# Kernel optimization log

Hardware: AMD Instinct MI355X
Metric: run time of the kernel (lower is better)

## Reference

```python
import jax, jax.numpy as jnp
import numpy as np

P_MIN = 0.8        # minimum cumulative probability mass kept per row
THRESHOLD = 1e-10  # drop matches with probability below this
EPS = 1e-6         # distance clamp (matches dist.clamp(min=1e-6) in backward)

B, N, M, D = 4, 4096, 4096, 3


def setup_inputs() -> dict:
    key = jax.random.key(0)
    kx, ky = jax.random.split(key)
    x = jax.random.normal(kx, (B, N, D), dtype=jnp.float32)
    y = jax.random.normal(ky, (B, M, D), dtype=jnp.float32)
    return {"x": x, "y": y}


def _pairwise_dist(x, y):
    # ||x_i - y_j|| via Gram trick; avoids materializing [B,N,M,D] diff tensor.
    sq = (
        jnp.sum(x * x, axis=-1)[:, :, None]
        + jnp.sum(y * y, axis=-1)[:, None, :]
        - 2.0 * jnp.einsum("bnd,bmd->bnm", x, y)
    )
    return jnp.sqrt(jnp.maximum(sq, EPS * EPS))  # [B, N, M]


def _sparse_match_weights(d):
    # Row-wise soft matching probabilities over targets j.
    p = jax.nn.softmax(-d, axis=-1)  # [B, N, M]
    # Keep the most-probable entries per row until cumulative mass reaches P_MIN
    # (the dense, jit-friendly equivalent of the COO compaction in the kernel).
    order = jnp.argsort(-p, axis=-1)
    p_sorted = jnp.take_along_axis(p, order, axis=-1)
    csum = jnp.cumsum(p_sorted, axis=-1)
    keep_sorted = (csum - p_sorted) < P_MIN  # include entry that crosses P_MIN
    inv = jnp.argsort(order, axis=-1)
    keep = jnp.take_along_axis(keep_sorted, inv, axis=-1)
    return jnp.where(keep & (p > THRESHOLD), p, 0.0)  # sparse COO values, dense layout


def reference(x, y):
    d = _pairwise_dist(x, y)                     # [B, N, M]
    w = jax.lax.stop_gradient(_sparse_match_weights(d))  # weights are constants in bwd
    loss = jnp.sum(w * d)                        # scalar matching loss
    return loss
```

## Files before the change

### kernel.cpp

```cpp
#include <hip/hip_runtime.h>


#define MCOLS 4096
#define KPT   64
#define WPB   4
#define P_MIN 0.8f

template <int CTRL, int RM, int BM, bool BC>
__device__ __forceinline__ float dpp_mov0(float x) {
    return __int_as_float(__builtin_amdgcn_update_dpp(
        0, __float_as_int(x), CTRL, RM, BM, BC));
}
__device__ __forceinline__ float dppSum(float v) {
    v += dpp_mov0<0x111, 0xF, 0xF, true >(v);
    v += dpp_mov0<0x112, 0xF, 0xF, true >(v);
    v += dpp_mov0<0x114, 0xF, 0xF, true >(v);
    v += dpp_mov0<0x118, 0xF, 0xF, true >(v);
    v += dpp_mov0<0x142, 0xA, 0xF, false>(v);
    v += dpp_mov0<0x143, 0xC, 0xF, false>(v);
    return __int_as_float(__builtin_amdgcn_readlane(__float_as_int(v), 63));
}
__device__ __forceinline__ void dppSum2(float& a, float& b) {
    a += dpp_mov0<0x111, 0xF, 0xF, true >(a); b += dpp_mov0<0x111, 0xF, 0xF, true >(b);
    a += dpp_mov0<0x112, 0xF, 0xF, true >(a); b += dpp_mov0<0x112, 0xF, 0xF, true >(b);
    a += dpp_mov0<0x114, 0xF, 0xF, true >(a); b += dpp_mov0<0x114, 0xF, 0xF, true >(b);
    a += dpp_mov0<0x118, 0xF, 0xF, true >(a); b += dpp_mov0<0x118, 0xF, 0xF, true >(b);
    a += dpp_mov0<0x142, 0xA, 0xF, false>(a); b += dpp_mov0<0x142, 0xA, 0xF, false>(b);
    a += dpp_mov0<0x143, 0xC, 0xF, false>(a); b += dpp_mov0<0x143, 0xC, 0xF, false>(b);
    a = __int_as_float(__builtin_amdgcn_readlane(__float_as_int(a), 63));
    b = __int_as_float(__builtin_amdgcn_readlane(__float_as_int(b), 63));
}
__device__ __forceinline__ float dppMax(float v) {
    v = fmaxf(v, dpp_mov0<0x111, 0xF, 0xF, true >(v));
    v = fmaxf(v, dpp_mov0<0x112, 0xF, 0xF, true >(v));
    v = fmaxf(v, dpp_mov0<0x114, 0xF, 0xF, true >(v));
    v = fmaxf(v, dpp_mov0<0x118, 0xF, 0xF, true >(v));
    v = fmaxf(v, dpp_mov0<0x142, 0xA, 0xF, false>(v));
    v = fmaxf(v, dpp_mov0<0x143, 0xC, 0xF, false>(v));
    return __int_as_float(__builtin_amdgcn_readlane(__float_as_int(v), 63));
}

__global__ __launch_bounds__(WPB * 64) void apml_row_wave(
        const float* __restrict__ x, const float* __restrict__ y,
        float* __restrict__ partial, float* __restrict__ out) {
    __shared__ __align__(16) float scomp[WPB * 256];
    __shared__ float wacc[WPB];

    const int tid  = threadIdx.x;
    const int wid  = tid >> 6;
    const int lane = tid & 63;
    const int row  = blockIdx.x * WPB + wid;
    const int b    = row >> 12;

    const float x0 = x[row * 3 + 0];
    const float x1 = x[row * 3 + 1];
    const float x2 = x[row * 3 + 2];
    const float* yb = y + (size_t)b * MCOLS * 3;

    float p[KPT];
    float zl = 0.0f;
    float pm0 = 0.0f, pm1 = 0.0f, pm2 = 0.0f, pm3 = 0.0f;
    #pragma unroll
    for (int k = 0; k < KPT; ++k) {
        const int j = k * 64 + lane;
        const float y0 = yb[j * 3 + 0];
        const float y1 = yb[j * 3 + 1];
        const float y2 = yb[j * 3 + 2];
        const float dx = x0 - y0, dy = x1 - y1, dz = x2 - y2;
        const float sq = fmaxf(dx * dx + dy * dy + dz * dz, 1e-12f);
        const float pk = __expf(-sqrtf(sq));
        p[k] = pk;
        zl  += pk;
        if      ((k & 3) == 0) pm0 = fmaxf(pm0, pk);
        else if ((k & 3) == 1) pm1 = fmaxf(pm1, pk);
        else if ((k & 3) == 2) pm2 = fmaxf(pm2, pk);
        else                   pm3 = fmaxf(pm3, pk);
    }
    const float Z    = dppSum(zl);
    const float pmax = dppMax(fmaxf(fmaxf(pm0, pm1), fmaxf(pm2, pm3)));
    const float target = P_MIN * Z;
    const float pTop = __uint_as_float(__float_as_uint(pmax) + 1u);

    float ssl = 0.0f, ssh = pTop;
    {
        float eGl = 16.0f * dppSum(p[0] + p[1] + p[2] + p[3]);
        float eGh = 0.0f;
        for (int it = 0; it < 3; ++it) {
            const float sB = 0.5f * (ssl + ssh);
            if (!(sB > ssl && sB < ssh)) break;
            float sA = ssl + (ssh - ssl) *
                       ((eGl - target) / fmaxf(eGl - eGh, 1e-30f));
            if (!(sA > ssl && sA < ssh)) sA = sB;
            const float t0 = fminf(sA, sB), t1 = fmaxf(sA, sB);

            float a0 = 0.0f, a1 = 0.0f;
            #pragma unroll
            for (int q = 0; q < 4; ++q) {
                a0 += (p[q] >= t0) ? p[q] : 0.0f;
                a1 += (p[q] >= t1) ? p[q] : 0.0f;
            }
            dppSum2(a0, a1);
            const float M0 = 16.0f * a0, M1 = 16.0f * a1;
            if      (M1 >= target) { ssl = t1; eGl = M1; }
            else if (M0 >= target) { ssl = t0; eGl = M0;
                                     ssh = t1; eGh = M1; }
            else                   { ssh = t0; eGh = M0; }
        }
    }

    float sl = 0.0f, sh = pTop;
    float Gl = Z,    Gh = 0.0f;
    int   Cl = MCOLS, Ch = 0;
    {
        float ml = 0.0f, mh = 0.0f;
        int   cl_ = 0,   ch_ = 0;
        #pragma unroll
        for (int k = 0; k < KPT; ++k) {
            const float pk = p[k];
            const bool gl = (pk >= ssl);
            const bool gh = (pk >= ssh);
            ml += gl ? pk : 0.0f; cl_ += (int)__popcll(__ballot(gl));
            mh += gh ? pk : 0.0f; ch_ += (int)__popcll(__ballot(gh));
        }
        dppSum2(ml, mh);
        if (ml >= target) { sl = ssl; Gl = ml; Cl = cl_; }
        else              { sh = ssl; Gh = ml; Ch = cl_; }
        if (mh >= target) { sl = ssh; Gl = mh; Cl = ch_; }
        else if (ssh < sh){ sh = ssh; Gh = mh; Ch = ch_; }
    }

    for (int it = 0; it < 10 && (Cl - Ch) > 256; ++it) {
        float s;
        if (it & 1) {
            s = 0.5f * (sl + sh);
        } else {
            const float den = fmaxf(Gl - Gh, 1e-30f);
            s = sl + (sh - sl) * ((Gl - target) / den);
        }
        if (!(s > sl && s < sh)) s = 0.5f * (sl + sh);
        if (!(s > sl && s < sh)) break;

        float m0 = 0.0f, m1 = 0.0f, m2 = 0.0f, m3 = 0.0f;
        int   c = 0;
        #pragma unroll
        for (int k = 0; k < KPT; k += 4) {
            const bool g0 = (p[k]     >= s);
            const bool g1 = (p[k + 1] >= s);
            const bool g2 = (p[k + 2] >= s);
            const bool g3 = (p[k + 3] >= s);
            m0 += g0 ? p[k]     : 0.0f; c += (int)__popcll(__ballot(g0));
            m1 += g1 ? p[k + 1] : 0.0f; c += (int)__popcll(__ballot(g1));
            m2 += g2 ? p[k + 2] : 0.0f; c += (int)__popcll(__ballot(g2));
            m3 += g3 ? p[k + 3] : 0.0f; c += (int)__popcll(__ballot(g3));
        }
        const float m = dppSum((m0 + m1) + (m2 + m3));
        if (m >= target) { sl = s; Gl = m; Cl = c; }
        else             { sh = s; Gh = m; Ch = c; }
    }

    int C = 0;
    #pragma unroll
    for (int k = 0; k < KPT; ++k) {
        const bool band = (p[k] >= sl) && (p[k] < sh);
        const unsigned long long mk = __ballot(band);
        if (band) {
            const unsigned mlo = (unsigned)mk, mhi = (unsigned)(mk >> 32);
            const int within = __builtin_amdgcn_mbcnt_hi(
                                   mhi, __builtin_amdgcn_mbcnt_lo(mlo, 0));
            const int pos = C + within;
            if (pos < 256) scomp[wid * 256 + pos] = p[k];
        }
        C += (int)__popcll(mk);
    }
    __builtin_amdgcn_s_waitcnt(0);
    float cp[4];
    bool  cv[4];
    #pragma unroll
    for (int q = 0; q < 4; ++q) {
        const int idx = q * 64 + lane;
        cv[q] = (idx < C) && (idx < 256);
        cp[q] = cv[q] ? scomp[wid * 256 + idx] : 0.0f;
    }

    float pstar, mb = 0.0f;
    int   cnt = 1;
    bool  haveTie;

    if (C > 256) {
        pstar = (sl > 0.0f) ? __uint_as_float(__float_as_uint(sl) - 1u) : 0.0f;
        haveTie = false;
    } else {
        float lo_s = sl, hi_s = sh, lo_G = Gl, hi_G = Gh;
        int   lo_C = Cl, hi_C = Ch;
        for (int it = 0; it < 6 && (lo_C - hi_C) > 2; ++it) {
            const float sB = 0.5f * (lo_s + hi_s);
            if (!(sB > lo_s && sB < hi_s)) break;
            float sA = lo_s + (hi_s - lo_s) *
                       ((lo_G - target) / fmaxf(lo_G - hi_G, 1e-30f));
            if (!(sA > lo_s && sA < hi_s)) sA = sB;
            const float t0 = fminf(sA, sB), t1 = fmaxf(sA, sB);

            float a0 = 0.0f, a1 = 0.0f;
            int   k0 = 0,    k1 = 0;
            #pragma unroll
            for (int q = 0; q < 4; ++q) {
                const bool g0 = cv[q] && (cp[q] >= t0);
                const bool g1 = cv[q] && (cp[q] >= t1);
                a0 += g0 ? cp[q] : 0.0f; k0 += (int)__popcll(__ballot(g0));
                a1 += g1 ? cp[q] : 0.0f; k1 += (int)__popcll(__ballot(g1));
            }
            dppSum2(a0, a1);
            const float M0 = Gh + a0, M1 = Gh + a1;
            const int   D0 = Ch + k0, D1 = Ch + k1;
            if      (M1 >= target) { lo_s = t1; lo_G = M1; lo_C = D1; }
            else if (M0 >= target) { lo_s = t0; lo_G = M0; lo_C = D0;
                                     hi_s = t1; hi_G = M1; hi_C = D1; }
            else                   { hi_s = t0; hi_G = M0; hi_C = D0; }
        }

        float scur = hi_s, M = hi_G;
        bool ok = false;
        pstar = lo_s;
        for (int e = 0; e < 16; ++e) {
            float vl = 0.0f;
            #pragma unroll
            for (int q = 0; q < 4; ++q)
                vl = fmaxf(vl, (cv[q] && cp[q] < scur) ? cp[q] : 0.0f);
            const float v = dppMax(vl);
            if (!(v > 0.0f)) break;
            int cvn = 0;
            #pragma unroll
            for (int q = 0; q < 4; ++q)
                cvn += (int)__popcll(__ballot(cv[q] && (cp[q] == v)));
            const float Mn = M + v * (float)cvn;
            if (Mn >= target) { pstar = v; mb = M; cnt = cvn; ok = true; break; }
            M = Mn; scur = v;
        }
        haveTie = ok;
        if (!ok) {
            pstar = (lo_s > 0.0f) ? __uint_as_float(__float_as_uint(lo_s) - 1u)
                                  : 0.0f;
        }
    }

    float s0 = 0.0f, s1 = 0.0f, s2 = 0.0f, s3 = 0.0f;
    #pragma unroll
    for (int k = 0; k < KPT; k += 4) {
        const float t0 = (p[k]     > pstar) ? p[k]     : 1.0f;
        const float t1 = (p[k + 1] > pstar) ? p[k + 1] : 1.0f;
        const float t2 = (p[k + 2] > pstar) ? p[k + 2] : 1.0f;
        const float t3 = (p[k + 3] > pstar) ? p[k + 3] : 1.0f;
        s0 += t0 * (-__logf(t0));
        s1 += t1 * (-__logf(t1));
        s2 += t2 * (-__logf(t2));
        s3 += t3 * (-__logf(t3));
    }
    const float spd = dppSum((s0 + s1) + (s2 + s3));

    if (lane == 0) {
        float tie = 0.0f;
        if (haveTie) {
            const float R = (target - mb) / pstar;
            int q = (int)ceilf(R);
            if (q < 1) q = 1;
            if (q > cnt) q = cnt;
            tie = (float)q * pstar * (-__logf(pstar));
        }
        wacc[wid] = (spd + tie) / Z;
    }
    __syncthreads();
    if (tid == 0) {
        const float v = wacc[0] + wacc[1] + wacc[2] + wacc[3];
        if (partial) partial[blockIdx.x] = v;
        else         atomicAdd(out, v);
    }
}

__global__ __launch_bounds__(1024) void apml_reduce(
        const float* __restrict__ partial, float* __restrict__ out, int n) {
    __shared__ float s[16];
    const int t = threadIdx.x;
    float a = 0.0f;
    #pragma unroll
    for (int q = 0; q < 4; ++q) {
        const int i = t * 4 + q;
        a += (i < n) ? partial[i] : 0.0f;
    }
    a = dppSum(a);
    if ((t & 63) == 0) s[t >> 6] = a;
    __syncthreads();
    if (t == 0) {
        float r = 0.0f;
        #pragma unroll
        for (int w = 0; w < 16; ++w) r += s[w];
        out[0] = r;
    }
}

extern "C" void kernel_launch(void* const* d_in, const int* in_sizes, int n_in,
                              void* d_out, int out_size, void* d_ws, size_t ws_size,
                              hipStream_t stream) {
    const float* x = (const float*)d_in[0];
    const float* y = (const float*)d_in[1];
    float* out = (float*)d_out;

    const int nrows = in_sizes[0] / 3;
    const int nblocks = nrows / WPB;

    if (d_ws && ws_size >= (size_t)nblocks * sizeof(float) && nblocks <= 4096) {
        float* partial = (float*)d_ws;
        apml_row_wave<<<nblocks, WPB * 64, 0, stream>>>(x, y, partial, out);
        apml_reduce<<<1, 1024, 0, stream>>>(partial, out, nblocks);
    } else {
        hipMemsetAsync(out, 0, sizeof(float), stream);
        apml_row_wave<<<nblocks, WPB * 64, 0, stream>>>(x, y, nullptr, out);
    }
}
```

Baseline: 166.3 us.

## Split each row across two cooperating waves with shared-memory reductions

Each row is now processed by a 128-thread block of two waves, each holding half the columns (32 values per lane instead of 64). All per-row reductions in the threshold search, band compaction and tie handling are combined across the two waves through shared memory and __syncthreads. The aim is to cut per-thread register pressure and raise occupancy and latency hiding. In exchange it adds many block barriers per row, doubles the block count, and enlarges the final reduction.

```diff
diff --git a/kernel.cpp b/kernel.cpp
--- a/kernel.cpp
+++ b/kernel.cpp
@@ -2,8 +2,7 @@
 
 
 #define MCOLS 4096
-#define KPT   64
-#define WPB   4
+#define KW    32
 #define P_MIN 0.8f
 
 template <int CTRL, int RM, int BM, bool BC>
@@ -40,16 +39,28 @@
     return __int_as_float(__builtin_amdgcn_readlane(__float_as_int(v), 63));
 }
 
-__global__ __launch_bounds__(WPB * 64) void apml_row_wave(
+__global__ __launch_bounds__(128) void apml_row_pair(
         const float* __restrict__ x, const float* __restrict__ y,
         float* __restrict__ partial, float* __restrict__ out) {
-    __shared__ __align__(16) float scomp[WPB * 256];
-    __shared__ float wacc[WPB];
+    __shared__ __align__(16) float scomp[256];
+    __shared__ float xf_set[4];
+    __shared__ float xf_g[2];
+    __shared__ float xf_warm[2][4];
+    __shared__ float xf_a0[4];
+    __shared__ int   xi_a0[4];
+    __shared__ float xf_A[2][2];
+    __shared__ int   xi_A[2][2];
+    __shared__ int   xi_bc[2];
+    __shared__ float xf_c1[2][4];
+    __shared__ int   xi_c1[2][4];
+    __shared__ float xf_c2v[2][2];
+    __shared__ int   xi_c2c[2][2];
+    __shared__ float xf_spd[2];
 
     const int tid  = threadIdx.x;
     const int wid  = tid >> 6;
     const int lane = tid & 63;
-    const int row  = blockIdx.x * WPB + wid;
+    const int row  = blockIdx.x;
     const int b    = row >> 12;
 
     const float x0 = x[row * 3 + 0];
@@ -57,12 +68,11 @@
     const float x2 = x[row * 3 + 2];
     const float* yb = y + (size_t)b * MCOLS * 3;
 
-    float p[KPT];
-    float zl = 0.0f;
-    float pm0 = 0.0f, pm1 = 0.0f, pm2 = 0.0f, pm3 = 0.0f;
-    #pragma unroll
-    for (int k = 0; k < KPT; ++k) {
-        const int j = k * 64 + lane;
+    float p[KW];
+    float zl = 0.0f, pm0 = 0.0f, pm1 = 0.0f;
+    #pragma unroll
+    for (int k = 0; k < KW; ++k) {
+        const int j = (wid * KW + k) * 64 + lane;
         const float y0 = yb[j * 3 + 0];
         const float y1 = yb[j * 3 + 1];
         const float y2 = yb[j * 3 + 2];
@@ -71,19 +81,23 @@
         const float pk = __expf(-sqrtf(sq));
         p[k] = pk;
         zl  += pk;
-        if      ((k & 3) == 0) pm0 = fmaxf(pm0, pk);
-        else if ((k & 3) == 1) pm1 = fmaxf(pm1, pk);
-        else if ((k & 3) == 2) pm2 = fmaxf(pm2, pk);
-        else                   pm3 = fmaxf(pm3, pk);
-    }
-    const float Z    = dppSum(zl);
-    const float pmax = dppMax(fmaxf(fmaxf(pm0, pm1), fmaxf(pm2, pm3)));
+        if (k & 1) pm1 = fmaxf(pm1, pk); else pm0 = fmaxf(pm0, pk);
+    }
+    const float Zw  = dppSum(zl);
+    const float pmw = dppMax(fmaxf(pm0, pm1));
+    if (lane == 0) { xf_set[wid * 2 + 0] = Zw; xf_set[wid * 2 + 1] = pmw; }
+    __syncthreads();
+    const float Z    = xf_set[0] + xf_set[2];
+    const float pmax = fmaxf(xf_set[1], xf_set[3]);
     const float target = P_MIN * Z;
     const float pTop = __uint_as_float(__float_as_uint(pmax) + 1u);
 
     float ssl = 0.0f, ssh = pTop;
     {
-        float eGl = 16.0f * dppSum(p[0] + p[1] + p[2] + p[3]);
+        const float gw = dppSum(p[0] + p[1] + p[2] + p[3]);
+        if (lane == 0) xf_g[wid] = gw;
+        __syncthreads();
+        float eGl = 8.0f * (xf_g[0] + xf_g[1]);
         float eGh = 0.0f;
         for (int it = 0; it < 3; ++it) {
             const float sB = 0.5f * (ssl + ssh);
@@ -100,7 +114,11 @@
                 a1 += (p[q] >= t1) ? p[q] : 0.0f;
             }
             dppSum2(a0, a1);
-            const float M0 = 16.0f * a0, M1 = 16.0f * a1;
+            if (lane == 0) { xf_warm[it & 1][wid * 2 + 0] = a0;
+                             xf_warm[it & 1][wid * 2 + 1] = a1; }
+            __syncthreads();
+            const float M0 = 8.0f * (xf_warm[it & 1][0] + xf_warm[it & 1][2]);
+            const float M1 = 8.0f * (xf_warm[it & 1][1] + xf_warm[it & 1][3]);
             if      (M1 >= target) { ssl = t1; eGl = M1; }
             else if (M0 >= target) { ssl = t0; eGl = M0;
                                      ssh = t1; eGh = M1; }
@@ -111,22 +129,30 @@
     float sl = 0.0f, sh = pTop;
     float Gl = Z,    Gh = 0.0f;
     int   Cl = MCOLS, Ch = 0;
+    int   clw = KW * 64, chw = 0;
     {
         float ml = 0.0f, mh = 0.0f;
-        int   cl_ = 0,   ch_ = 0;
+        int   clo = 0,   cho = 0;
         #pragma unroll
-        for (int k = 0; k < KPT; ++k) {
+        for (int k = 0; k < KW; ++k) {
             const float pk = p[k];
             const bool gl = (pk >= ssl);
             const bool gh = (pk >= ssh);
-            ml += gl ? pk : 0.0f; cl_ += (int)__popcll(__ballot(gl));
-            mh += gh ? pk : 0.0f; ch_ += (int)__popcll(__ballot(gh));
+            ml += gl ? pk : 0.0f; clo += (int)__popcll(__ballot(gl));
+            mh += gh ? pk : 0.0f; cho += (int)__popcll(__ballot(gh));
         }
         dppSum2(ml, mh);
-        if (ml >= target) { sl = ssl; Gl = ml; Cl = cl_; }
-        else              { sh = ssl; Gh = ml; Ch = cl_; }
-        if (mh >= target) { sl = ssh; Gl = mh; Cl = ch_; }
-        else if (ssh < sh){ sh = ssh; Gh = mh; Ch = ch_; }
+        if (lane == 0) { xf_a0[wid * 2 + 0] = ml; xf_a0[wid * 2 + 1] = mh;
+                         xi_a0[wid * 2 + 0] = clo; xi_a0[wid * 2 + 1] = cho; }
+        __syncthreads();
+        const float MlC = xf_a0[0] + xf_a0[2];
+        const float MhC = xf_a0[1] + xf_a0[3];
+        const int   ClC = xi_a0[0] + xi_a0[2];
+        const int   ChC = xi_a0[1] + xi_a0[3];
+        if (MlC >= target) { sl = ssl; Gl = MlC; Cl = ClC; clw = clo; }
+        else               { sh = ssl; Gh = MlC; Ch = ClC; chw = clo; }
+        if (MhC >= target) { sl = ssh; Gl = MhC; Cl = ChC; clw = cho; }
+        else if (ssh < sh) { sh = ssh; Gh = MhC; Ch = ChC; chw = cho; }
     }
 
     for (int it = 0; it < 10 && (Cl - Ch) > 256; ++it) {
@@ -140,46 +166,50 @@
         if (!(s > sl && s < sh)) s = 0.5f * (sl + sh);
         if (!(s > sl && s < sh)) break;
 
-        float m0 = 0.0f, m1 = 0.0f, m2 = 0.0f, m3 = 0.0f;
+        float m0 = 0.0f, m1 = 0.0f;
         int   c = 0;
         #pragma unroll
-        for (int k = 0; k < KPT; k += 4) {
+        for (int k = 0; k < KW; k += 2) {
             const bool g0 = (p[k]     >= s);
             const bool g1 = (p[k + 1] >= s);
-            const bool g2 = (p[k + 2] >= s);
-            const bool g3 = (p[k + 3] >= s);
             m0 += g0 ? p[k]     : 0.0f; c += (int)__popcll(__ballot(g0));
             m1 += g1 ? p[k + 1] : 0.0f; c += (int)__popcll(__ballot(g1));
-            m2 += g2 ? p[k + 2] : 0.0f; c += (int)__popcll(__ballot(g2));
-            m3 += g3 ? p[k + 3] : 0.0f; c += (int)__popcll(__ballot(g3));
-        }
-        const float m = dppSum((m0 + m1) + (m2 + m3));
-        if (m >= target) { sl = s; Gl = m; Cl = c; }
-        else             { sh = s; Gh = m; Ch = c; }
-    }
-
-    int C = 0;
-    #pragma unroll
-    for (int k = 0; k < KPT; ++k) {
+        }
+        const float mw = dppSum(m0 + m1);
+        if (lane == 0) { xf_A[it & 1][wid] = mw; xi_A[it & 1][wid] = c; }
+        __syncthreads();
+        const float m = xf_A[it & 1][0] + xf_A[it & 1][1];
+        const int   cC = xi_A[it & 1][0] + xi_A[it & 1][1];
+        if (m >= target) { sl = s; Gl = m; Cl = cC; clw = c; }
+        else             { sh = s; Gh = m; Ch = cC; chw = c; }
+    }
+
+    const int bc_own = clw - chw;
+    if (lane == 0) xi_bc[wid] = bc_own;
+    __syncthreads();
+    const int C    = xi_bc[0] + xi_bc[1];
+    int       ofs  = (wid == 0) ? 0 : xi_bc[0];
+    #pragma unroll
+    for (int k = 0; k < KW; ++k) {
         const bool band = (p[k] >= sl) && (p[k] < sh);
         const unsigned long long mk = __ballot(band);
         if (band) {
             const unsigned mlo = (unsigned)mk, mhi = (unsigned)(mk >> 32);
             const int within = __builtin_amdgcn_mbcnt_hi(
                                    mhi, __builtin_amdgcn_mbcnt_lo(mlo, 0));
-            const int pos = C + within;
-            if (pos < 256) scomp[wid * 256 + pos] = p[k];
-        }
-        C += (int)__popcll(mk);
-    }
-    __builtin_amdgcn_s_waitcnt(0);
-    float cp[4];
-    bool  cv[4];
-    #pragma unroll
-    for (int q = 0; q < 4; ++q) {
-        const int idx = q * 64 + lane;
+            const int pos = ofs + within;
+            if (pos < 256) scomp[pos] = p[k];
+        }
+        ofs += (int)__popcll(mk);
+    }
+    __syncthreads();
+    float cp[2];
+    bool  cv[2];
+    #pragma unroll
+    for (int q = 0; q < 2; ++q) {
+        const int idx = q * 128 + wid * 64 + lane;
         cv[q] = (idx < C) && (idx < 256);
-        cp[q] = cv[q] ? scomp[wid * 256 + idx] : 0.0f;
+        cp[q] = cv[q] ? scomp[idx] : 0.0f;
     }
 
     float pstar, mb = 0.0f;
@@ -203,15 +233,22 @@
             float a0 = 0.0f, a1 = 0.0f;
             int   k0 = 0,    k1 = 0;
             #pragma unroll
-            for (int q = 0; q < 4; ++q) {
+            for (int q = 0; q < 2; ++q) {
                 const bool g0 = cv[q] && (cp[q] >= t0);
                 const bool g1 = cv[q] && (cp[q] >= t1);
                 a0 += g0 ? cp[q] : 0.0f; k0 += (int)__popcll(__ballot(g0));
                 a1 += g1 ? cp[q] : 0.0f; k1 += (int)__popcll(__ballot(g1));
             }
             dppSum2(a0, a1);
-            const float M0 = Gh + a0, M1 = Gh + a1;
-            const int   D0 = Ch + k0, D1 = Ch + k1;
+            if (lane == 0) { xf_c1[it & 1][wid * 2 + 0] = a0;
+                             xf_c1[it & 1][wid * 2 + 1] = a1;
+                             xi_c1[it & 1][wid * 2 + 0] = k0;
+                             xi_c1[it & 1][wid * 2 + 1] = k1; }
+            __syncthreads();
+            const float M0 = Gh + xf_c1[it & 1][0] + xf_c1[it & 1][2];
+            const float M1 = Gh + xf_c1[it & 1][1] + xf_c1[it & 1][3];
+            const int   D0 = Ch + xi_c1[it & 1][0] + xi_c1[it & 1][2];
+            const int   D1 = Ch + xi_c1[it & 1][1] + xi_c1[it & 1][3];
             if      (M1 >= target) { lo_s = t1; lo_G = M1; lo_C = D1; }
             else if (M0 >= target) { lo_s = t0; lo_G = M0; lo_C = D0;
                                      hi_s = t1; hi_G = M1; hi_C = D1; }
@@ -224,14 +261,20 @@
         for (int e = 0; e < 16; ++e) {
             float vl = 0.0f;
             #pragma unroll
-            for (int q = 0; q < 4; ++q)
+            for (int q = 0; q < 2; ++q)
                 vl = fmaxf(vl, (cv[q] && cp[q] < scur) ? cp[q] : 0.0f);
-            const float v = dppMax(vl);
+            const float vw = dppMax(vl);
+            if (lane == 0) xf_c2v[e & 1][wid] = vw;
+            __syncthreads();
+            const float v = fmaxf(xf_c2v[e & 1][0], xf_c2v[e & 1][1]);
             if (!(v > 0.0f)) break;
-            int cvn = 0;
+            int cvo = 0;
             #pragma unroll
-            for (int q = 0; q < 4; ++q)
-                cvn += (int)__popcll(__ballot(cv[q] && (cp[q] == v)));
+            for (int q = 0; q < 2; ++q)
+                cvo += (int)__popcll(__ballot(cv[q] && (cp[q] == v)));
+            if (lane == 0) xi_c2c[e & 1][wid] = cvo;
+            __syncthreads();
+            const int cvn = xi_c2c[e & 1][0] + xi_c2c[e & 1][1];
             const float Mn = M + v * (float)cvn;
             if (Mn >= target) { pstar = v; mb = M; cnt = cvn; ok = true; break; }
             M = Mn; scur = v;
@@ -243,21 +286,20 @@
         }
     }
 
-    float s0 = 0.0f, s1 = 0.0f, s2 = 0.0f, s3 = 0.0f;
-    #pragma unroll
-    for (int k = 0; k < KPT; k += 4) {
+    float s0 = 0.0f, s1 = 0.0f;
+    #pragma unroll
+    for (int k = 0; k < KW; k += 2) {
         const float t0 = (p[k]     > pstar) ? p[k]     : 1.0f;
         const float t1 = (p[k + 1] > pstar) ? p[k + 1] : 1.0f;
-        const float t2 = (p[k + 2] > pstar) ? p[k + 2] : 1.0f;
-        const float t3 = (p[k + 3] > pstar) ? p[k + 3] : 1.0f;
         s0 += t0 * (-__logf(t0));
         s1 += t1 * (-__logf(t1));
-        s2 += t2 * (-__logf(t2));
-        s3 += t3 * (-__logf(t3));
-    }
-    const float spd = dppSum((s0 + s1) + (s2 + s3));
-
-    if (lane == 0) {
+    }
+    const float spdw = dppSum(s0 + s1);
+    if (lane == 0) xf_spd[wid] = spdw;
+    __syncthreads();
+
+    if (tid == 0) {
+        const float spd = xf_spd[0] + xf_spd[1];
         float tie = 0.0f;
         if (haveTie) {
             const float R = (target - mb) / pstar;
@@ -266,12 +308,8 @@
             if (q > cnt) q = cnt;
             tie = (float)q * pstar * (-__logf(pstar));
         }
-        wacc[wid] = (spd + tie) / Z;
-    }
-    __syncthreads();
-    if (tid == 0) {
-        const float v = wacc[0] + wacc[1] + wacc[2] + wacc[3];
-        if (partial) partial[blockIdx.x] = v;
+        const float v = (spd + tie) / Z;
+        if (partial) partial[row] = v;
         else         atomicAdd(out, v);
     }
 }
@@ -282,8 +320,8 @@
     const int t = threadIdx.x;
     float a = 0.0f;
     #pragma unroll
-    for (int q = 0; q < 4; ++q) {
-        const int i = t * 4 + q;
+    for (int q = 0; q < 16; ++q) {
+        const int i = t * 16 + q;
         a += (i < n) ? partial[i] : 0.0f;
     }
     a = dppSum(a);
@@ -305,14 +343,15 @@
     float* out = (float*)d_out;
 
     const int nrows = in_sizes[0] / 3;
-    const int nblocks = nrows / WPB;
-
-    if (d_ws && ws_size >= (size_t)nblocks * sizeof(float) && nblocks <= 4096) {
+
+    const size_t part_bytes = (size_t)nrows * sizeof(float);
+
+    if (d_ws && ws_size >= part_bytes && nrows <= 16384) {
         float* partial = (float*)d_ws;
-        apml_row_wave<<<nblocks, WPB * 64, 0, stream>>>(x, y, partial, out);
-        apml_reduce<<<1, 1024, 0, stream>>>(partial, out, nblocks);
+        apml_row_pair<<<nrows, 128, 0, stream>>>(x, y, partial, out);
+        apml_reduce<<<1, 1024, 0, stream>>>(partial, out, nrows);
     } else {
         hipMemsetAsync(out, 0, sizeof(float), stream);
-        apml_row_wave<<<nblocks, WPB * 64, 0, stream>>>(x, y, nullptr, out);
-    }
-}
+        apml_row_pair<<<nrows, 128, 0, stream>>>(x, y, nullptr, out);
+    }
+}
```

Result: slower. 183.3 us (+10.2%).
